# Kernel tuning notes

Hardware: AMD Instinct MI355X
Metric: run time of the kernel (lower is better)

Reference implementation:

```python
import jax, jax.numpy as jnp
import numpy as np

T, D, E, H, O = 65536, 256, 8, 512, 256
TOP_P = 0.7


def setup_inputs() -> dict:
    key = jax.random.key(0)
    ks = jax.random.split(key, 7)
    s = 0.02
    return {
        "x": jax.random.normal(ks[0], (T, D), dtype=jnp.float32),
        "gate_w": jax.random.normal(ks[1], (D, E), dtype=jnp.float32) * s,
        "gate_b": jnp.zeros((E,), dtype=jnp.float32),
        "w1": jax.random.normal(ks[2], (E, D, H), dtype=jnp.float32) * s,
        "b1": jnp.zeros((E, H), dtype=jnp.float32),
        "w2": jax.random.normal(ks[3], (E, H, O), dtype=jnp.float32) * s,
        "b2": jnp.zeros((E, O), dtype=jnp.float32),
    }


def top_sample(probs, top_p):
    # sort descending, cumsum, keep while cumulative prob <= top_p (always keep top-1)
    order = jnp.argsort(-probs, axis=-1)                       # [T, E]
    probs_sorted = jnp.take_along_axis(probs, order, axis=-1)
    cum = jnp.cumsum(probs_sorted, axis=-1)
    mask = cum <= top_p
    mask = mask.at[:, 0].set(True)
    inv = jnp.argsort(order, axis=-1)                          # unsort permutation
    return jnp.take_along_axis(mask, inv, axis=-1)             # [T, E] bool


def reference(x, gate_w, gate_b, w1, b1, w2, b2):
    logits = x @ gate_w + gate_b                               # [T, E]
    probs = jax.nn.softmax(logits, axis=-1)
    routing_loss = jnp.mean(-jnp.sum(probs * jnp.log(probs + 1e-8), axis=-1))
    expert_mask = top_sample(probs, TOP_P)                     # [T, E]

    # dense per-expert MLP over the entire batch (faithful to original)
    h = jax.nn.gelu(jnp.einsum('td,edh->teh', x, w1) + b1, approximate=False)
    expert_outputs = jnp.einsum('teh,eho->teo', h, w2) + b2    # [T, E, O]

    mask_probs = probs * expert_mask.astype(probs.dtype)
    weights = mask_probs / jnp.sum(mask_probs, axis=-1, keepdims=True)  # [T, E]
    output = jnp.einsum('teo,te->to', expert_outputs, weights)          # [T, O]
    return output, routing_loss
```

## Files before the change

### kernel.cpp

```cpp
#include <hip/hip_runtime.h>
#include <math.h>

#define TT 65536
#define DD 256
#define EE 8
#define HH 512
#define OO 256
#define NN 4096

typedef unsigned int u32;
typedef unsigned short u16;
typedef __attribute__((ext_vector_type(4))) float f32x4;
typedef __attribute__((ext_vector_type(16))) float f32x16;
typedef __attribute__((ext_vector_type(2))) u32 u32x2;
typedef __attribute__((ext_vector_type(4))) u32 u32x4;
typedef __attribute__((ext_vector_type(8))) __bf16 bf16x8;

__device__ __forceinline__ u16 f2bf(float f) {
    u32 u = __builtin_bit_cast(u32, f);
    u32 r = (u + 0x7fffu + ((u >> 16) & 1u)) >> 16;
    return (u16)r;
}

__device__ __forceinline__ u32 cvt_pk_bf16(float lo, float hi) {
    u32 r;
    asm("v_cvt_pk_bf16_f32 %0, %1, %2" : "=v"(r) : "v"(lo), "v"(hi));
    return r;
}

__device__ __forceinline__ bf16x8 ld_frag(const void* p) {
    u32x4 v = *(const u32x4*)p;
    return __builtin_bit_cast(bf16x8, v);
}

__device__ __forceinline__ float gelu_fast(float v) {
    float t = v * v;
    float u = __builtin_fmaf(t, -0.1029479f, -2.3022075f);
    float z = v * u;
    float e = __builtin_amdgcn_exp2f(z);
    return v * __builtin_amdgcn_rcpf(1.0f + e);
}

__global__ __launch_bounds__(256) void k_conv_w1(const float* __restrict__ w1, u16* __restrict__ w1s) {
    int i = blockIdx.x * 256 + threadIdx.x;
    int j = i & 15, l = (i >> 4) & 31, kb = (i >> 9) & 15, nb = i >> 13;
    int n = nb * 32 + l, k = kb * 16 + j;
    int e = n >> 9, h = n & 511;
    w1s[i] = f2bf(w1[(size_t)e * 131072 + (size_t)k * 512 + h]);
}
__global__ __launch_bounds__(256) void k_conv_w2(const float* __restrict__ w2, u16* __restrict__ w2s) {
    int i = blockIdx.x * 256 + threadIdx.x;
    int j = i & 15, l = (i >> 4) & 31, kb2 = (i >> 9) & 255, ob = i >> 17;
    int o = ob * 32 + l, k2 = kb2 * 16 + j;
    int e = k2 >> 9, h = k2 & 511;
    w2s[i] = f2bf(w2[(size_t)e * 131072 + (size_t)h * 256 + o]);
}

__global__ __launch_bounds__(256) void k_gating(const float* __restrict__ x,
                                                const float* __restrict__ gw,
                                                const float* __restrict__ gb,
                                                float* __restrict__ wt,
                                                double* __restrict__ part) {
    __shared__ float gws[DD * EE];
    __shared__ float gbs[EE];
    __shared__ double red[256];
    int tid = threadIdx.x;
    for (int i = tid; i < DD * EE; i += 256) gws[i] = gw[i];
    if (tid < EE) gbs[tid] = gb[tid];
    __syncthreads();

    int t = blockIdx.x * 256 + tid;
    double l[EE];
#pragma unroll
    for (int e = 0; e < EE; ++e) l[e] = (double)gbs[e];

    const f32x4* xr = (const f32x4*)(x + (size_t)t * DD);
    for (int d4 = 0; d4 < DD / 4; ++d4) {
        f32x4 xv = xr[d4];
#pragma unroll
        for (int j = 0; j < 4; ++j) {
            double xs = (double)xv[j];
            int d = d4 * 4 + j;
#pragma unroll
            for (int e = 0; e < EE; ++e) l[e] += xs * (double)gws[d * EE + e];
        }
    }
    double mx = l[0];
#pragma unroll
    for (int e = 1; e < EE; ++e) mx = l[e] > mx ? l[e] : mx;
    double p[EE], s = 0.0;
#pragma unroll
    for (int e = 0; e < EE; ++e) { p[e] = exp(l[e] - mx); s += p[e]; }
    double inv = 1.0 / s;
    double ent = 0.0;
#pragma unroll
    for (int e = 0; e < EE; ++e) { p[e] *= inv; ent += p[e] * log(p[e] + 1e-8); }

    bool mask[EE];
#pragma unroll
    for (int e = 0; e < EE; ++e) {
        double c = 0.0; int rk = 0;
#pragma unroll
        for (int f = 0; f < EE; ++f) {
            bool before = (p[f] > p[e]) || (p[f] == p[e] && f < e);
            if (before) { c += p[f]; rk++; }
        }
        c += p[e];
        mask[e] = (c <= 0.7) || (rk == 0);
    }
    double ms = 0.0;
#pragma unroll
    for (int e = 0; e < EE; ++e) if (mask[e]) ms += p[e];
    double inv2 = 1.0 / ms;
#pragma unroll
    for (int e = 0; e < EE; ++e) wt[(size_t)e * TT + t] = (float)(mask[e] ? p[e] * inv2 : 0.0);

    red[tid] = -ent;
    __syncthreads();
    for (int st = 128; st > 0; st >>= 1) {
        if (tid < st) red[tid] += red[tid + st];
        __syncthreads();
    }
    if (tid == 0) part[blockIdx.x] = red[0];
}

__global__ __launch_bounds__(256) void k_final(const double* __restrict__ part, float* __restrict__ loss) {
    __shared__ double red[256];
    int tid = threadIdx.x;
    red[tid] = part[tid];
    __syncthreads();
    for (int st = 128; st > 0; st >>= 1) {
        if (tid < st) red[tid] += red[tid + st];
        __syncthreads();
    }
    if (tid == 0) loss[0] = (float)(red[0] / (double)TT);
}

__global__ __launch_bounds__(512, 4) void k_moe(const float* __restrict__ x,
                                                const u16* __restrict__ w1s,
                                                const u16* __restrict__ w2s,
                                                const float* __restrict__ b1,
                                                const float* __restrict__ b2,
                                                const float* __restrict__ wtg,
                                                float* __restrict__ out) {
    __shared__ __align__(16) unsigned char smem[67584];
    unsigned char* Hs = smem + 32768;
    float* wts = (float*)(smem + 65536);

    const int tid = threadIdx.x;
    const int wid = tid >> 6;
    const int lane = tid & 63;
    const int l31 = lane & 31;
    const int lg2 = lane >> 5;
    const int t0 = blockIdx.x * 64;
    const int lfrag = l31 * 16 + lg2 * 8;

    {
        const float* xb = x + (size_t)t0 * DD;
#pragma unroll
        for (int i = 0; i < 4; ++i) {
            int L = i * 8192 + tid * 16;
            int row = L >> 9, elem = (L & 511) >> 1;
            const float* src = xb + (size_t)row * DD + elem;
            f32x4 a = *(const f32x4*)src;
            f32x4 b = *(const f32x4*)(src + 4);
            u32x4 o;
            o.x = cvt_pk_bf16(a[0], a[1]); o.y = cvt_pk_bf16(a[2], a[3]);
            o.z = cvt_pk_bf16(b[0], b[1]); o.w = cvt_pk_bf16(b[2], b[3]);
            *(u32x4*)(smem + (L ^ ((row & 15) << 4))) = o;
        }
    }
    wts[tid] = wtg[(size_t)(tid >> 6) * TT + t0 + (tid & 63)];
    __syncthreads();

    f32x16 oacc[2];
    oacc[0] = (f32x16)0.0f;
    oacc[1] = (f32x16)0.0f;

    const int tokA = l31, tokB = 32 + l31;
    const int rbA = tokA * 512 + lg2 * 16, rszA = (tokA & 15) << 4;
    const int rbB = tokB * 512 + lg2 * 16, rszB = (tokB & 15) << 4;

#pragma unroll 1
    for (int c = 0; c < 16; ++c) {
        const int e = c >> 1;
        {
            f32x16 hf0 = (f32x16)0.0f, hf1 = (f32x16)0.0f;
            const u16* w1p = w1s + ((size_t)((c * 8 + wid) * 16)) * 512 + lfrag;
            bf16x8 A[4];
            A[0] = ld_frag(w1p);
            A[1] = ld_frag(w1p + 512);
            A[2] = ld_frag(w1p + 1024);
            A[3] = ld_frag(w1p + 1536);
#pragma unroll 4
            for (int ks = 0; ks < 16; ++ks) {
                bf16x8 ac = A[ks & 3];
                if (ks < 12) A[ks & 3] = ld_frag(w1p + (ks + 4) * 512);
                bf16x8 b0 = ld_frag(smem + ((rbA + ks * 32) ^ rszA));
                bf16x8 b1 = ld_frag(smem + ((rbB + ks * 32) ^ rszB));
                hf0 = __builtin_amdgcn_mfma_f32_32x32x16_bf16(ac, b0, hf0, 0, 0, 0);
                hf1 = __builtin_amdgcn_mfma_f32_32x32x16_bf16(ac, b1, hf1, 0, 0, 0);
            }
            const float* b1p = b1 + c * 256 + wid * 32 + lg2 * 4;
            float wgtA = wts[e * 64 + tokA];
            float wgtB = wts[e * 64 + tokB];
#pragma unroll
            for (int q = 0; q < 4; ++q) {
                f32x4 bb = *(const f32x4*)(b1p + q * 8);
                float g0[4], g1[4];
#pragma unroll
                for (int r = 0; r < 4; ++r) {
                    g0[r] = gelu_fast(hf0[q * 4 + r] + bb[r]) * wgtA;
                    g1[r] = gelu_fast(hf1[q * 4 + r] + bb[r]) * wgtB;
                }
                u32x2 pk0, pk1;
                pk0.x = cvt_pk_bf16(g0[0], g0[1]); pk0.y = cvt_pk_bf16(g0[2], g0[3]);
                pk1.x = cvt_pk_bf16(g1[0], g1[1]); pk1.y = cvt_pk_bf16(g1[2], g1[3]);
                int hb = (wid * 32 + q * 8 + lg2 * 4) * 2;
                *(u32x2*)(Hs + ((tokA * 512 + hb) ^ rszA)) = pk0;
                *(u32x2*)(Hs + ((tokB * 512 + hb) ^ rszB)) = pk1;
            }
        }
        __syncthreads();
        {
            const u16* w2p = w2s + ((size_t)(wid * 256 + c * 16)) * 512 + lfrag;
            bf16x8 B[4];
            B[0] = ld_frag(w2p);
            B[1] = ld_frag(w2p + 512);
            B[2] = ld_frag(w2p + 1024);
            B[3] = ld_frag(w2p + 1536);
#pragma unroll 4
            for (int ks = 0; ks < 16; ++ks) {
                bf16x8 bc = B[ks & 3];
                if (ks < 12) B[ks & 3] = ld_frag(w2p + (ks + 4) * 512);
                bf16x8 A0 = ld_frag(Hs + ((rbA + ks * 32) ^ rszA));
                bf16x8 A1 = ld_frag(Hs + ((rbB + ks * 32) ^ rszB));
                oacc[0] = __builtin_amdgcn_mfma_f32_32x32x16_bf16(A0, bc, oacc[0], 0, 0, 0);
                oacc[1] = __builtin_amdgcn_mfma_f32_32x32x16_bf16(A1, bc, oacc[1], 0, 0, 0);
            }
        }
        __syncthreads();
    }

    {
        int o = wid * 32 + l31;
        float b2v[EE];
#pragma unroll
        for (int e = 0; e < EE; ++e) b2v[e] = b2[e * OO + o];
#pragma unroll
        for (int m = 0; m < 2; ++m) {
#pragma unroll
            for (int r = 0; r < 16; ++r) {
                int tok = m * 32 + (r & 3) + 8 * (r >> 2) + 4 * lg2;
                float wb = 0.f;
#pragma unroll
                for (int e = 0; e < EE; ++e) wb += wts[e * 64 + tok] * b2v[e];
                out[(size_t)(t0 + tok) * OO + o] = oacc[m][r] + wb;
            }
        }
    }
}

extern "C" void kernel_launch(void* const* d_in, const int* in_sizes, int n_in,
                              void* d_out, int out_size, void* d_ws, size_t ws_size,
                              hipStream_t stream) {
    const float* x  = (const float*)d_in[0];
    const float* gw = (const float*)d_in[1];
    const float* gb = (const float*)d_in[2];
    const float* w1 = (const float*)d_in[3];
    const float* b1 = (const float*)d_in[4];
    const float* w2 = (const float*)d_in[5];
    const float* b2 = (const float*)d_in[6];
    float* out = (float*)d_out;

    char* ws = (char*)d_ws;
    u16* w1s    = (u16*)(ws);
    u16* w2s    = (u16*)(ws + 2097152);
    float* wt   = (float*)(ws + 4194304);
    double* prt = (double*)(ws + 6291456);

    k_conv_w1<<<(EE * HH * DD) / 256, 256, 0, stream>>>(w1, w1s);
    k_conv_w2<<<(OO * NN) / 256, 256, 0, stream>>>(w2, w2s);
    k_gating<<<TT / 256, 256, 0, stream>>>(x, gw, gb, wt, prt);
    k_moe<<<TT / 64, 512, 0, stream>>>(x, w1s, w2s, b1, b2, wt, out);
    k_final<<<1, 256, 0, stream>>>(prt, out + (size_t)TT * OO);
}
```

Measured before the change: 377.8 us.

## Use 4-wave blocks with halved H chunks and 2x2 output tiles per wave

The MoE block drops from 8 waves to 4 waves per 64-token tile. The hidden dimension is processed in 32 chunks of 128 instead of 16 chunks of 256, which halves the H staging buffer in shared memory. Each wave now accumulates a 64x64 output tile (2x2 MFMA tiles), so each H fragment read from shared memory feeds two MFMAs. This cuts LDS traffic per MFMA and lowers shared memory per block, but there are twice as many barrier-separated chunks and fewer waves to hide latency. The larger accumulator set also raises register pressure.

```diff
diff --git a/kernel.cpp b/kernel.cpp
--- a/kernel.cpp
+++ b/kernel.cpp
@@ -136,16 +136,16 @@
     if (tid == 0) loss[0] = (float)(red[0] / (double)TT);
 }
 
-__global__ __launch_bounds__(512, 4) void k_moe(const float* __restrict__ x,
+__global__ __launch_bounds__(256, 3) void k_moe(const float* __restrict__ x,
                                                 const u16* __restrict__ w1s,
                                                 const u16* __restrict__ w2s,
                                                 const float* __restrict__ b1,
                                                 const float* __restrict__ b2,
                                                 const float* __restrict__ wtg,
                                                 float* __restrict__ out) {
-    __shared__ __align__(16) unsigned char smem[67584];
+    __shared__ __align__(16) unsigned char smem[51200];
     unsigned char* Hs = smem + 32768;
-    float* wts = (float*)(smem + 65536);
+    float* wts = (float*)(smem + 49152);
 
     const int tid = threadIdx.x;
     const int wid = tid >> 6;
@@ -158,8 +158,8 @@
     {
         const float* xb = x + (size_t)t0 * DD;
 #pragma unroll
-        for (int i = 0; i < 4; ++i) {
-            int L = i * 8192 + tid * 16;
+        for (int i = 0; i < 8; ++i) {
+            int L = i * 4096 + tid * 16;
             int row = L >> 9, elem = (L & 511) >> 1;
             const float* src = xb + (size_t)row * DD + elem;
             f32x4 a = *(const f32x4*)src;
@@ -171,22 +171,27 @@
         }
     }
     wts[tid] = wtg[(size_t)(tid >> 6) * TT + t0 + (tid & 63)];
-    __syncthreads();
-
-    f32x16 oacc[2];
-    oacc[0] = (f32x16)0.0f;
-    oacc[1] = (f32x16)0.0f;
+    wts[tid + 256] = wtg[(size_t)((tid + 256) >> 6) * TT + t0 + (tid & 63)];
+    __syncthreads();
+
+    f32x16 oacc[2][2];
+#pragma unroll
+    for (int m = 0; m < 2; ++m)
+#pragma unroll
+        for (int n = 0; n < 2; ++n) oacc[m][n] = (f32x16)0.0f;
 
     const int tokA = l31, tokB = 32 + l31;
-    const int rbA = tokA * 512 + lg2 * 16, rszA = (tokA & 15) << 4;
-    const int rbB = tokB * 512 + lg2 * 16, rszB = (tokB & 15) << 4;
+    const int xbA = tokA * 512 + lg2 * 16, rszA = (tokA & 15) << 4;
+    const int xbB = tokB * 512 + lg2 * 16, rszB = (tokB & 15) << 4;
+    const int hbA = tokA * 256 + lg2 * 16;
+    const int hbB = tokB * 256 + lg2 * 16;
 
 #pragma unroll 1
-    for (int c = 0; c < 16; ++c) {
-        const int e = c >> 1;
+    for (int c = 0; c < 32; ++c) {
+        const int e = c >> 2;
         {
             f32x16 hf0 = (f32x16)0.0f, hf1 = (f32x16)0.0f;
-            const u16* w1p = w1s + ((size_t)((c * 8 + wid) * 16)) * 512 + lfrag;
+            const u16* w1p = w1s + ((size_t)((c * 4 + wid) * 16)) * 512 + lfrag;
             bf16x8 A[4];
             A[0] = ld_frag(w1p);
             A[1] = ld_frag(w1p + 512);
@@ -196,12 +201,12 @@
             for (int ks = 0; ks < 16; ++ks) {
                 bf16x8 ac = A[ks & 3];
                 if (ks < 12) A[ks & 3] = ld_frag(w1p + (ks + 4) * 512);
-                bf16x8 b0 = ld_frag(smem + ((rbA + ks * 32) ^ rszA));
-                bf16x8 b1 = ld_frag(smem + ((rbB + ks * 32) ^ rszB));
+                bf16x8 b0 = ld_frag(smem + ((xbA + ks * 32) ^ rszA));
+                bf16x8 b1 = ld_frag(smem + ((xbB + ks * 32) ^ rszB));
                 hf0 = __builtin_amdgcn_mfma_f32_32x32x16_bf16(ac, b0, hf0, 0, 0, 0);
                 hf1 = __builtin_amdgcn_mfma_f32_32x32x16_bf16(ac, b1, hf1, 0, 0, 0);
             }
-            const float* b1p = b1 + c * 256 + wid * 32 + lg2 * 4;
+            const float* b1p = b1 + c * 128 + wid * 32 + lg2 * 4;
             float wgtA = wts[e * 64 + tokA];
             float wgtB = wts[e * 64 + tokB];
 #pragma unroll
@@ -217,33 +222,40 @@
                 pk0.x = cvt_pk_bf16(g0[0], g0[1]); pk0.y = cvt_pk_bf16(g0[2], g0[3]);
                 pk1.x = cvt_pk_bf16(g1[0], g1[1]); pk1.y = cvt_pk_bf16(g1[2], g1[3]);
                 int hb = (wid * 32 + q * 8 + lg2 * 4) * 2;
-                *(u32x2*)(Hs + ((tokA * 512 + hb) ^ rszA)) = pk0;
-                *(u32x2*)(Hs + ((tokB * 512 + hb) ^ rszB)) = pk1;
+                *(u32x2*)(Hs + ((tokA * 256 + hb) ^ rszA)) = pk0;
+                *(u32x2*)(Hs + ((tokB * 256 + hb) ^ rszB)) = pk1;
             }
         }
         __syncthreads();
         {
-            const u16* w2p = w2s + ((size_t)(wid * 256 + c * 16)) * 512 + lfrag;
-            bf16x8 B[4];
-            B[0] = ld_frag(w2p);
-            B[1] = ld_frag(w2p + 512);
-            B[2] = ld_frag(w2p + 1024);
-            B[3] = ld_frag(w2p + 1536);
+            const u16* w2p0 = w2s + ((size_t)(wid * 2) * 256 + c * 8) * 512 + lfrag;
+            const u16* w2p1 = w2p0 + (size_t)256 * 512;
+            bf16x8 B0[2], B1[2];
+            B0[0] = ld_frag(w2p0);
+            B1[0] = ld_frag(w2p1);
+            B0[1] = ld_frag(w2p0 + 512);
+            B1[1] = ld_frag(w2p1 + 512);
 #pragma unroll 4
-            for (int ks = 0; ks < 16; ++ks) {
-                bf16x8 bc = B[ks & 3];
-                if (ks < 12) B[ks & 3] = ld_frag(w2p + (ks + 4) * 512);
-                bf16x8 A0 = ld_frag(Hs + ((rbA + ks * 32) ^ rszA));
-                bf16x8 A1 = ld_frag(Hs + ((rbB + ks * 32) ^ rszB));
-                oacc[0] = __builtin_amdgcn_mfma_f32_32x32x16_bf16(A0, bc, oacc[0], 0, 0, 0);
-                oacc[1] = __builtin_amdgcn_mfma_f32_32x32x16_bf16(A1, bc, oacc[1], 0, 0, 0);
-            }
-        }
-        __syncthreads();
-    }
-
-    {
-        int o = wid * 32 + l31;
+            for (int ks = 0; ks < 8; ++ks) {
+                bf16x8 bc0 = B0[ks & 1], bc1 = B1[ks & 1];
+                if (ks < 6) {
+                    B0[ks & 1] = ld_frag(w2p0 + (ks + 2) * 512);
+                    B1[ks & 1] = ld_frag(w2p1 + (ks + 2) * 512);
+                }
+                bf16x8 A0 = ld_frag(Hs + ((hbA + ks * 32) ^ rszA));
+                bf16x8 A1 = ld_frag(Hs + ((hbB + ks * 32) ^ rszB));
+                oacc[0][0] = __builtin_amdgcn_mfma_f32_32x32x16_bf16(A0, bc0, oacc[0][0], 0, 0, 0);
+                oacc[0][1] = __builtin_amdgcn_mfma_f32_32x32x16_bf16(A0, bc1, oacc[0][1], 0, 0, 0);
+                oacc[1][0] = __builtin_amdgcn_mfma_f32_32x32x16_bf16(A1, bc0, oacc[1][0], 0, 0, 0);
+                oacc[1][1] = __builtin_amdgcn_mfma_f32_32x32x16_bf16(A1, bc1, oacc[1][1], 0, 0, 0);
+            }
+        }
+        __syncthreads();
+    }
+
+#pragma unroll
+    for (int n = 0; n < 2; ++n) {
+        int o = wid * 64 + n * 32 + l31;
         float b2v[EE];
 #pragma unroll
         for (int e = 0; e < EE; ++e) b2v[e] = b2[e * OO + o];
@@ -255,7 +267,7 @@
                 float wb = 0.f;
 #pragma unroll
                 for (int e = 0; e < EE; ++e) wb += wts[e * 64 + tok] * b2v[e];
-                out[(size_t)(t0 + tok) * OO + o] = oacc[m][r] + wb;
+                out[(size_t)(t0 + tok) * OO + o] = oacc[m][n][r] + wb;
             }
         }
     }
@@ -282,6 +294,6 @@
     k_conv_w1<<<(EE * HH * DD) / 256, 256, 0, stream>>>(w1, w1s);
     k_conv_w2<<<(OO * NN) / 256, 256, 0, stream>>>(w2, w2s);
     k_gating<<<TT / 256, 256, 0, stream>>>(x, gw, gb, wt, prt);
-    k_moe<<<TT / 64, 512, 0, stream>>>(x, w1s, w2s, b1, b2, wt, out);
+    k_moe<<<TT / 64, 256, 0, stream>>>(x, w1s, w2s, b1, b2, wt, out);
     k_final<<<1, 256, 0, stream>>>(prt, out + (size_t)TT * OO);
 }
```

Result: slower. 698.1 us (+84.8%).

## Remap warps to 32-token by 64-column tiles to halve LDS fragment loads

Applied to the files above, without the earlier changes.

Each warp now handles one 32-token group and two 32-wide weight column strips, instead of all 64 tokens and one column strip. Each LDS activation fragment then feeds two MFMAs with different weight fragments. This halves LDS reads per MFMA but doubles the global/L2 weight fragment traffic per warp, since each block now loads its weights twice across the two token groups. The weight prefetch depth is reduced from 4 to 2 to keep register use in check.

```diff
diff --git a/kernel.cpp b/kernel.cpp
--- a/kernel.cpp
+++ b/kernel.cpp
@@ -152,6 +152,8 @@
     const int lane = tid & 63;
     const int l31 = lane & 31;
     const int lg2 = lane >> 5;
+    const int tg = wid & 1;
+    const int strip = wid >> 1;
     const int t0 = blockIdx.x * 64;
     const int lfrag = l31 * 16 + lg2 * 8;
 
@@ -177,86 +179,86 @@
     oacc[0] = (f32x16)0.0f;
     oacc[1] = (f32x16)0.0f;
 
-    const int tokA = l31, tokB = 32 + l31;
-    const int rbA = tokA * 512 + lg2 * 16, rszA = (tokA & 15) << 4;
-    const int rbB = tokB * 512 + lg2 * 16, rszB = (tokB & 15) << 4;
+    const int xrow = tg * 32 + l31;
+    const int xb0 = xrow * 512 + lg2 * 16;
+    const int xsz = (xrow & 15) << 4;
 
 #pragma unroll 1
     for (int c = 0; c < 16; ++c) {
         const int e = c >> 1;
         {
             f32x16 hf0 = (f32x16)0.0f, hf1 = (f32x16)0.0f;
-            const u16* w1p = w1s + ((size_t)((c * 8 + wid) * 16)) * 512 + lfrag;
-            bf16x8 A[4];
-            A[0] = ld_frag(w1p);
-            A[1] = ld_frag(w1p + 512);
-            A[2] = ld_frag(w1p + 1024);
-            A[3] = ld_frag(w1p + 1536);
+            const u16* w1p0 = w1s + ((size_t)((c * 8 + strip * 2 + 0) * 16)) * 512 + lfrag;
+            const u16* w1p1 = w1s + ((size_t)((c * 8 + strip * 2 + 1) * 16)) * 512 + lfrag;
+            bf16x8 A0[2], A1[2];
+            A0[0] = ld_frag(w1p0);       A0[1] = ld_frag(w1p0 + 512);
+            A1[0] = ld_frag(w1p1);       A1[1] = ld_frag(w1p1 + 512);
 #pragma unroll 4
             for (int ks = 0; ks < 16; ++ks) {
-                bf16x8 ac = A[ks & 3];
-                if (ks < 12) A[ks & 3] = ld_frag(w1p + (ks + 4) * 512);
-                bf16x8 b0 = ld_frag(smem + ((rbA + ks * 32) ^ rszA));
-                bf16x8 b1 = ld_frag(smem + ((rbB + ks * 32) ^ rszB));
-                hf0 = __builtin_amdgcn_mfma_f32_32x32x16_bf16(ac, b0, hf0, 0, 0, 0);
-                hf1 = __builtin_amdgcn_mfma_f32_32x32x16_bf16(ac, b1, hf1, 0, 0, 0);
+                bf16x8 ac0 = A0[ks & 1], ac1 = A1[ks & 1];
+                if (ks < 14) {
+                    A0[ks & 1] = ld_frag(w1p0 + (ks + 2) * 512);
+                    A1[ks & 1] = ld_frag(w1p1 + (ks + 2) * 512);
+                }
+                bf16x8 b = ld_frag(smem + ((xb0 + ks * 32) ^ xsz));
+                hf0 = __builtin_amdgcn_mfma_f32_32x32x16_bf16(ac0, b, hf0, 0, 0, 0);
+                hf1 = __builtin_amdgcn_mfma_f32_32x32x16_bf16(ac1, b, hf1, 0, 0, 0);
             }
-            const float* b1p = b1 + c * 256 + wid * 32 + lg2 * 4;
-            float wgtA = wts[e * 64 + tokA];
-            float wgtB = wts[e * 64 + tokB];
-#pragma unroll
-            for (int q = 0; q < 4; ++q) {
-                f32x4 bb = *(const f32x4*)(b1p + q * 8);
-                float g0[4], g1[4];
-#pragma unroll
-                for (int r = 0; r < 4; ++r) {
-                    g0[r] = gelu_fast(hf0[q * 4 + r] + bb[r]) * wgtA;
-                    g1[r] = gelu_fast(hf1[q * 4 + r] + bb[r]) * wgtB;
+            float wgt = wts[e * 64 + xrow];
+#pragma unroll
+            for (int t = 0; t < 2; ++t) {
+                const float* b1p = b1 + c * 256 + strip * 64 + t * 32 + lg2 * 4;
+                const f32x16& hf = t ? hf1 : hf0;
+#pragma unroll
+                for (int q = 0; q < 4; ++q) {
+                    f32x4 bb = *(const f32x4*)(b1p + q * 8);
+                    float g[4];
+#pragma unroll
+                    for (int r = 0; r < 4; ++r)
+                        g[r] = gelu_fast(hf[q * 4 + r] + bb[r]) * wgt;
+                    u32x2 pk;
+                    pk.x = cvt_pk_bf16(g[0], g[1]);
+                    pk.y = cvt_pk_bf16(g[2], g[3]);
+                    int hb = (strip * 64 + t * 32 + q * 8 + lg2 * 4) * 2;
+                    *(u32x2*)(Hs + ((xrow * 512 + hb) ^ xsz)) = pk;
                 }
-                u32x2 pk0, pk1;
-                pk0.x = cvt_pk_bf16(g0[0], g0[1]); pk0.y = cvt_pk_bf16(g0[2], g0[3]);
-                pk1.x = cvt_pk_bf16(g1[0], g1[1]); pk1.y = cvt_pk_bf16(g1[2], g1[3]);
-                int hb = (wid * 32 + q * 8 + lg2 * 4) * 2;
-                *(u32x2*)(Hs + ((tokA * 512 + hb) ^ rszA)) = pk0;
-                *(u32x2*)(Hs + ((tokB * 512 + hb) ^ rszB)) = pk1;
             }
         }
         __syncthreads();
         {
-            const u16* w2p = w2s + ((size_t)(wid * 256 + c * 16)) * 512 + lfrag;
-            bf16x8 B[4];
-            B[0] = ld_frag(w2p);
-            B[1] = ld_frag(w2p + 512);
-            B[2] = ld_frag(w2p + 1024);
-            B[3] = ld_frag(w2p + 1536);
+            const u16* w2p0 = w2s + ((size_t)((strip * 2 + 0) * 256 + c * 16)) * 512 + lfrag;
+            const u16* w2p1 = w2s + ((size_t)((strip * 2 + 1) * 256 + c * 16)) * 512 + lfrag;
+            bf16x8 B0[2], B1[2];
+            B0[0] = ld_frag(w2p0);       B0[1] = ld_frag(w2p0 + 512);
+            B1[0] = ld_frag(w2p1);       B1[1] = ld_frag(w2p1 + 512);
 #pragma unroll 4
             for (int ks = 0; ks < 16; ++ks) {
-                bf16x8 bc = B[ks & 3];
-                if (ks < 12) B[ks & 3] = ld_frag(w2p + (ks + 4) * 512);
-                bf16x8 A0 = ld_frag(Hs + ((rbA + ks * 32) ^ rszA));
-                bf16x8 A1 = ld_frag(Hs + ((rbB + ks * 32) ^ rszB));
-                oacc[0] = __builtin_amdgcn_mfma_f32_32x32x16_bf16(A0, bc, oacc[0], 0, 0, 0);
-                oacc[1] = __builtin_amdgcn_mfma_f32_32x32x16_bf16(A1, bc, oacc[1], 0, 0, 0);
+                bf16x8 bc0 = B0[ks & 1], bc1 = B1[ks & 1];
+                if (ks < 14) {
+                    B0[ks & 1] = ld_frag(w2p0 + (ks + 2) * 512);
+                    B1[ks & 1] = ld_frag(w2p1 + (ks + 2) * 512);
+                }
+                bf16x8 Ah = ld_frag(Hs + ((xb0 + ks * 32) ^ xsz));
+                oacc[0] = __builtin_amdgcn_mfma_f32_32x32x16_bf16(Ah, bc0, oacc[0], 0, 0, 0);
+                oacc[1] = __builtin_amdgcn_mfma_f32_32x32x16_bf16(Ah, bc1, oacc[1], 0, 0, 0);
             }
         }
         __syncthreads();
     }
 
-    {
-        int o = wid * 32 + l31;
+#pragma unroll
+    for (int n = 0; n < 2; ++n) {
+        int o = strip * 64 + n * 32 + l31;
         float b2v[EE];
 #pragma unroll
         for (int e = 0; e < EE; ++e) b2v[e] = b2[e * OO + o];
 #pragma unroll
-        for (int m = 0; m < 2; ++m) {
-#pragma unroll
-            for (int r = 0; r < 16; ++r) {
-                int tok = m * 32 + (r & 3) + 8 * (r >> 2) + 4 * lg2;
-                float wb = 0.f;
-#pragma unroll
-                for (int e = 0; e < EE; ++e) wb += wts[e * 64 + tok] * b2v[e];
-                out[(size_t)(t0 + tok) * OO + o] = oacc[m][r] + wb;
-            }
+        for (int r = 0; r < 16; ++r) {
+            int tok = tg * 32 + (r & 3) + 8 * (r >> 2) + 4 * lg2;
+            float wb = 0.f;
+#pragma unroll
+            for (int e = 0; e < EE; ++e) wb += wts[e * 64 + tok] * b2v[e];
+            out[(size_t)(t0 + tok) * OO + o] = oacc[n][r] + wb;
         }
     }
 }
```

Result: slower. 478.5 us (+26.7%).
